# Kernel optimization log

Hardware: AMD Instinct MI355X
Metric: run time of the kernel (lower is better)

The kernel has to match this reference:

```python
import jax, jax.numpy as jnp
import numpy as np

B, N = 8192, 512
WEIGHT_THRESHOLD = 0.0
EPS = 1e-5


def setup_inputs() -> dict:
    key = jax.random.key(0)
    k1, k2, k3 = jax.random.split(key, 3)
    src_points = jax.random.normal(k1, (B, N, 3), dtype=jnp.float32)
    tgt_points = jax.random.normal(k2, (B, N, 3), dtype=jnp.float32)
    weights = jax.random.uniform(k3, (B, N), dtype=jnp.float32)
    return {"src_points": src_points, "tgt_points": tgt_points, "weights": weights}


def _weighted_procrustes(src, tgt, w):
    # threshold + normalize weights  (B, N)
    w = jnp.where(w < WEIGHT_THRESHOLD, jnp.zeros_like(w), w)
    w = w / (jnp.sum(w, axis=1, keepdims=True) + EPS)
    w3 = w[..., None]                                   # (B, N, 1)
    # weighted centroids (B, 1, 3)
    src_c = jnp.sum(w3 * src, axis=1, keepdims=True)
    tgt_c = jnp.sum(w3 * tgt, axis=1, keepdims=True)
    src0 = src - src_c
    tgt0 = tgt - tgt_c
    # weighted covariance H = src0^T (w * tgt0)  -> (B, 3, 3)
    H = jnp.einsum("bni,bnj->bij", src0, w3 * tgt0)
    U, S, Vh = jnp.linalg.svd(H)
    V = jnp.swapaxes(Vh, -1, -2)
    Ut = jnp.swapaxes(U, -1, -2)
    # reflection correction: diag(1, 1, sign(det(V U^T)))
    det = jnp.linalg.det(jnp.matmul(V, Ut))             # (B,)
    ones = jnp.ones((src.shape[0], 2), dtype=src.dtype)
    d = jnp.concatenate([ones, jnp.sign(det)[:, None]], axis=1)  # (B, 3)
    R = jnp.einsum("bij,bj,bjk->bik", V, d, Ut)         # (B, 3, 3)
    t = tgt_c[:, 0, :] - jnp.einsum("bij,bj->bi", R, src_c[:, 0, :])  # (B, 3)
    return R, t


def reference(src_points, tgt_points, weights):
    return _weighted_procrustes(src_points, tgt_points, weights)
```

## Files before the change

### kernel.cpp

```cpp
#include <hip/hip_runtime.h>

#define NPTS 512
#define BLOCK 256
#define BLOCK_S 64
#define XPS 68

#define GLOBAL_AS(p) ((const __attribute__((address_space(1))) void*)(p))
#define LDS_AS(p)    ((__attribute__((address_space(3))) void*)(p))

__global__ __launch_bounds__(BLOCK) void wproc_moments(
    const float* __restrict__ src,
    const float* __restrict__ tgt,
    const float* __restrict__ wts,
    float* __restrict__ ws)
{
    const int b = blockIdx.x;
    const int t = threadIdx.x;
    const int wave = t >> 6, lane = t & 63;

    __shared__ __align__(16) char smem[4 * 16 * XPS * 4];
    __shared__ float red[4][16];

    const char* sb = (const char*)(src + (size_t)b * (NPTS * 3));
    const char* tb = (const char*)(tgt + (size_t)b * (NPTS * 3));
    const char* wb = (const char*)(wts + (size_t)b * NPTS);

    for (int c = wave; c < 14; c += 4) {
        const char* g;
        if (c < 6)       g = sb + (size_t)c * 1024;
        else if (c < 12) g = tb + (size_t)(c - 6) * 1024;
        else             g = wb + (size_t)(c - 12) * 1024;
        __builtin_amdgcn_global_load_lds(
            GLOBAL_AS(g + lane * 16),
            LDS_AS(smem + c * 1024),
            16, 0, 2);
    }
    __syncthreads();

    const float* s_s = (const float*)smem;
    const float* s_t = (const float*)(smem + 6144);
    const float* s_w = (const float*)(smem + 12288);

    float acc[16];
    #pragma unroll
    for (int i = 0; i < 16; ++i) acc[i] = 0.f;

    #pragma unroll
    for (int k = 0; k < 2; ++k) {
        const int p = t + k * 256;
        float w = s_w[p];
        w = (w < 0.f) ? 0.f : w;
        const float sx = s_s[3 * p + 0], sy = s_s[3 * p + 1], sz = s_s[3 * p + 2];
        const float tx = s_t[3 * p + 0], ty = s_t[3 * p + 1], tz = s_t[3 * p + 2];
        acc[0] += w;
        acc[1] += w * sx; acc[2] += w * sy; acc[3] += w * sz;
        acc[4] += w * tx; acc[5] += w * ty; acc[6] += w * tz;
        const float wsx = w * sx, wsy = w * sy, wsz = w * sz;
        acc[7]  += wsx * tx; acc[8]  += wsx * ty; acc[9]  += wsx * tz;
        acc[10] += wsy * tx; acc[11] += wsy * ty; acc[12] += wsy * tz;
        acc[13] += wsz * tx; acc[14] += wsz * ty; acc[15] += wsz * tz;
    }
    __syncthreads();

    float (*xp)[16][XPS] = (float (*)[16][XPS])smem;
    #pragma unroll
    for (int m = 0; m < 16; ++m) xp[wave][m][lane] = acc[m];

    {
        const int m = lane & 15, q = lane >> 4;
        const float4* row = (const float4*)&xp[wave][m][0] + 4 * q;
        float4 a0 = row[0], a1 = row[1], a2 = row[2], a3 = row[3];
        a0.x += a1.x; a0.y += a1.y; a0.z += a1.z; a0.w += a1.w;
        a2.x += a3.x; a2.y += a3.y; a2.z += a3.z; a2.w += a3.w;
        a0.x += a2.x; a0.y += a2.y; a0.z += a2.z; a0.w += a2.w;
        float v = (a0.x + a0.y) + (a0.z + a0.w);
        v += __shfl_xor(v, 16, 64);
        v += __shfl_xor(v, 32, 64);
        if (q == 0) red[wave][m] = v;
    }
    __syncthreads();

    if (t < 16) {
        ws[(size_t)b * 16 + t] =
            (red[0][t] + red[1][t]) + (red[2][t] + red[3][t]);
    }
}

__global__ __launch_bounds__(BLOCK_S) void wproc_solve(
    const float* __restrict__ ws,
    float* __restrict__ out,
    int B)
{
    const int b = blockIdx.x * BLOCK_S + threadIdx.x;
    if (b >= B) return;

    double m[16];
    #pragma unroll
    for (int i = 0; i < 16; ++i) m[i] = (double)ws[(size_t)b * 16 + i];

    const double T = m[0] + 1e-5;
    const double f = 2.0 - m[0] / T;
    const double cs[3] = { m[1] / T, m[2] / T, m[3] / T };
    const double ct[3] = { m[4] / T, m[5] / T, m[6] / T };
    double H[3][3];
    #pragma unroll
    for (int i = 0; i < 3; ++i)
        #pragma unroll
        for (int j = 0; j < 3; ++j)
            H[i][j] = m[7 + i * 3 + j] / T - f * cs[i] * ct[j];

    double A[3][3];
    #pragma unroll
    for (int i = 0; i < 3; ++i)
        #pragma unroll
        for (int j = 0; j < 3; ++j)
            A[i][j] = H[0][i] * H[0][j] + H[1][i] * H[1][j] + H[2][i] * H[2][j];

    double V[3][3] = { {1, 0, 0}, {0, 1, 0}, {0, 0, 1} };
    #pragma unroll
    for (int sweep = 0; sweep < 5; ++sweep) {
        #pragma unroll
        for (int pair = 0; pair < 3; ++pair) {
            const int p = (pair == 2) ? 1 : 0;
            const int q = (pair == 0) ? 1 : 2;
            const double apq = A[p][q];
            const double theta = (A[q][q] - A[p][p]) / (2.0 * apq);
            const double tt = ((theta >= 0.0) ? 1.0 : -1.0)
                            / (fabs(theta) + sqrt(theta * theta + 1.0));
            double c  = 1.0 / sqrt(tt * tt + 1.0);
            double sn = tt * c;
            const bool zero = (apq == 0.0);
            c  = zero ? 1.0 : c;
            sn = zero ? 0.0 : sn;
            #pragma unroll
            for (int k = 0; k < 3; ++k) {
                const double akp = A[k][p], akq = A[k][q];
                A[k][p] = c * akp - sn * akq;
                A[k][q] = sn * akp + c * akq;
            }
            #pragma unroll
            for (int k = 0; k < 3; ++k) {
                const double apk = A[p][k], aqk = A[q][k];
                A[p][k] = c * apk - sn * aqk;
                A[q][k] = sn * apk + c * aqk;
            }
            #pragma unroll
            for (int k = 0; k < 3; ++k) {
                const double vkp = V[k][p], vkq = V[k][q];
                V[k][p] = c * vkp - sn * vkq;
                V[k][q] = sn * vkp + c * vkq;
            }
        }
    }

    double lam[3] = { A[0][0], A[1][1], A[2][2] };
    #define CSWAP(a_, b_) do {                                                \
        const bool sw_ = lam[a_] < lam[b_];                                   \
        const double tl_ = lam[a_];                                           \
        lam[a_] = sw_ ? lam[b_] : lam[a_];                                    \
        lam[b_] = sw_ ? tl_ : lam[b_];                                        \
        _Pragma("unroll")                                                     \
        for (int k = 0; k < 3; ++k) {                                         \
            const double tv_ = V[k][a_];                                      \
            V[k][a_] = sw_ ? V[k][b_] : V[k][a_];                             \
            V[k][b_] = sw_ ? tv_ : V[k][b_];                                  \
        }                                                                     \
    } while (0)
    CSWAP(0, 1); CSWAP(0, 2); CSWAP(1, 2);
    #undef CSWAP

    const double v1[3] = { V[0][0], V[1][0], V[2][0] };
    const double v2[3] = { V[0][1], V[1][1], V[2][1] };
    const double v3[3] = { v1[1] * v2[2] - v1[2] * v2[1],
                           v1[2] * v2[0] - v1[0] * v2[2],
                           v1[0] * v2[1] - v1[1] * v2[0] };

    double u1[3], u2[3], u3[3];
    #pragma unroll
    for (int i = 0; i < 3; ++i)
        u1[i] = H[i][0] * v1[0] + H[i][1] * v1[1] + H[i][2] * v1[2];
    double n1 = sqrt(u1[0] * u1[0] + u1[1] * u1[1] + u1[2] * u1[2]);
    n1 = (n1 > 1e-30) ? n1 : 1e-30;
    #pragma unroll
    for (int i = 0; i < 3; ++i) u1[i] /= n1;

    #pragma unroll
    for (int i = 0; i < 3; ++i)
        u2[i] = H[i][0] * v2[0] + H[i][1] * v2[1] + H[i][2] * v2[2];
    const double d12 = u1[0] * u2[0] + u1[1] * u2[1] + u1[2] * u2[2];
    #pragma unroll
    for (int i = 0; i < 3; ++i) u2[i] -= d12 * u1[i];
    double n2 = sqrt(u2[0] * u2[0] + u2[1] * u2[1] + u2[2] * u2[2]);
    n2 = (n2 > 1e-30) ? n2 : 1e-30;
    #pragma unroll
    for (int i = 0; i < 3; ++i) u2[i] /= n2;

    u3[0] = u1[1] * u2[2] - u1[2] * u2[1];
    u3[1] = u1[2] * u2[0] - u1[0] * u2[2];
    u3[2] = u1[0] * u2[1] - u1[1] * u2[0];

    double R[3][3];
    #pragma unroll
    for (int i = 0; i < 3; ++i)
        #pragma unroll
        for (int j = 0; j < 3; ++j)
            R[i][j] = v1[i] * u1[j] + v2[i] * u2[j] + v3[i] * u3[j];

    double tv[3];
    #pragma unroll
    for (int i = 0; i < 3; ++i)
        tv[i] = ct[i] - (R[i][0] * cs[0] + R[i][1] * cs[1] + R[i][2] * cs[2]);

    float* outR = out + (size_t)b * 9;
    #pragma unroll
    for (int i = 0; i < 3; ++i)
        #pragma unroll
        for (int j = 0; j < 3; ++j)
            outR[i * 3 + j] = (float)R[i][j];
    float* outT = out + (size_t)B * 9 + (size_t)b * 3;
    #pragma unroll
    for (int i = 0; i < 3; ++i) outT[i] = (float)tv[i];
}

extern "C" void kernel_launch(void* const* d_in, const int* in_sizes, int n_in,
                              void* d_out, int out_size, void* d_ws, size_t ws_size,
                              hipStream_t stream) {
    const float* src = (const float*)d_in[0];
    const float* tgt = (const float*)d_in[1];
    const float* wts = (const float*)d_in[2];
    float* out = (float*)d_out;
    float* ws = (float*)d_ws;
    const int B = out_size / 12;

    wproc_moments<<<B, BLOCK, 0, stream>>>(src, tgt, wts, ws);
    wproc_solve<<<(B + BLOCK_S - 1) / BLOCK_S, BLOCK_S, 0, stream>>>(ws, out, B);
}
```

Measured before the change: 134.6 us.

## Use persistent blocks with double-buffered async LDS staging in moments kernel

Replaces the one-block-per-batch moments kernel with a fixed grid of persistent blocks that loop over batches. Each iteration issues async global-to-LDS loads for the next batch into a second buffer while reducing the current one, so load latency overlaps compute. The cost is fewer resident blocks and extra LDS per block. A single barrier per iteration guards buffer reuse, and the xp scratch is reused between iterations, which raises questions about whether the LDS hazards are fully covered.

```diff
diff --git a/kernel.cpp b/kernel.cpp
--- a/kernel.cpp
+++ b/kernel.cpp
@@ -4,6 +4,7 @@
 #define BLOCK 256
 #define BLOCK_S 64
 #define XPS 68
+#define GRID_M 768
 
 #define GLOBAL_AS(p) ((const __attribute__((address_space(1))) void*)(p))
 #define LDS_AS(p)    ((__attribute__((address_space(3))) void*)(p))
@@ -12,77 +13,86 @@
     const float* __restrict__ src,
     const float* __restrict__ tgt,
     const float* __restrict__ wts,
-    float* __restrict__ ws)
+    float* __restrict__ ws,
+    int B)
 {
-    const int b = blockIdx.x;
     const int t = threadIdx.x;
     const int wave = t >> 6, lane = t & 63;
 
-    __shared__ __align__(16) char smem[4 * 16 * XPS * 4];
-    __shared__ float red[4][16];
-
-    const char* sb = (const char*)(src + (size_t)b * (NPTS * 3));
-    const char* tb = (const char*)(tgt + (size_t)b * (NPTS * 3));
-    const char* wb = (const char*)(wts + (size_t)b * NPTS);
-
-    for (int c = wave; c < 14; c += 4) {
-        const char* g;
-        if (c < 6)       g = sb + (size_t)c * 1024;
-        else if (c < 12) g = tb + (size_t)(c - 6) * 1024;
-        else             g = wb + (size_t)(c - 12) * 1024;
-        __builtin_amdgcn_global_load_lds(
-            GLOBAL_AS(g + lane * 16),
-            LDS_AS(smem + c * 1024),
-            16, 0, 2);
-    }
+    __shared__ __align__(16) char buf[2][14336];
+    __shared__ __align__(16) float xp[4][16][XPS];
+    __shared__ float red[2][4][16];
+
+    auto stage = [&](int b, char* dst) {
+        const char* sb = (const char*)(src + (size_t)b * (NPTS * 3));
+        const char* tb = (const char*)(tgt + (size_t)b * (NPTS * 3));
+        const char* wb = (const char*)(wts + (size_t)b * NPTS);
+        for (int c = wave; c < 14; c += 4) {
+            const char* g;
+            if (c < 6)       g = sb + (size_t)c * 1024;
+            else if (c < 12) g = tb + (size_t)(c - 6) * 1024;
+            else             g = wb + (size_t)(c - 12) * 1024;
+            __builtin_amdgcn_global_load_lds(
+                GLOBAL_AS(g + lane * 16),
+                LDS_AS(dst + c * 1024),
+                16, 0, 2);
+        }
+    };
+
+    int b = blockIdx.x;
+    if (b < B) stage(b, buf[0]);
     __syncthreads();
 
-    const float* s_s = (const float*)smem;
-    const float* s_t = (const float*)(smem + 6144);
-    const float* s_w = (const float*)(smem + 12288);
-
-    float acc[16];
-    #pragma unroll
-    for (int i = 0; i < 16; ++i) acc[i] = 0.f;
-
-    #pragma unroll
-    for (int k = 0; k < 2; ++k) {
-        const int p = t + k * 256;
-        float w = s_w[p];
-        w = (w < 0.f) ? 0.f : w;
-        const float sx = s_s[3 * p + 0], sy = s_s[3 * p + 1], sz = s_s[3 * p + 2];
-        const float tx = s_t[3 * p + 0], ty = s_t[3 * p + 1], tz = s_t[3 * p + 2];
-        acc[0] += w;
-        acc[1] += w * sx; acc[2] += w * sy; acc[3] += w * sz;
-        acc[4] += w * tx; acc[5] += w * ty; acc[6] += w * tz;
-        const float wsx = w * sx, wsy = w * sy, wsz = w * sz;
-        acc[7]  += wsx * tx; acc[8]  += wsx * ty; acc[9]  += wsx * tz;
-        acc[10] += wsy * tx; acc[11] += wsy * ty; acc[12] += wsy * tz;
-        acc[13] += wsz * tx; acc[14] += wsz * ty; acc[15] += wsz * tz;
-    }
-    __syncthreads();
-
-    float (*xp)[16][XPS] = (float (*)[16][XPS])smem;
-    #pragma unroll
-    for (int m = 0; m < 16; ++m) xp[wave][m][lane] = acc[m];
-
-    {
-        const int m = lane & 15, q = lane >> 4;
-        const float4* row = (const float4*)&xp[wave][m][0] + 4 * q;
-        float4 a0 = row[0], a1 = row[1], a2 = row[2], a3 = row[3];
-        a0.x += a1.x; a0.y += a1.y; a0.z += a1.z; a0.w += a1.w;
-        a2.x += a3.x; a2.y += a3.y; a2.z += a3.z; a2.w += a3.w;
-        a0.x += a2.x; a0.y += a2.y; a0.z += a2.z; a0.w += a2.w;
-        float v = (a0.x + a0.y) + (a0.z + a0.w);
-        v += __shfl_xor(v, 16, 64);
-        v += __shfl_xor(v, 32, 64);
-        if (q == 0) red[wave][m] = v;
-    }
-    __syncthreads();
-
-    if (t < 16) {
-        ws[(size_t)b * 16 + t] =
-            (red[0][t] + red[1][t]) + (red[2][t] + red[3][t]);
+    int p = 0;
+    for (; b < B; b += GRID_M, p ^= 1) {
+        const int bn = b + GRID_M;
+        if (bn < B) stage(bn, buf[p ^ 1]);
+
+        const float* s_s = (const float*)(buf[p]);
+        const float* s_t = (const float*)(buf[p] + 6144);
+        const float* s_w = (const float*)(buf[p] + 12288);
+
+        float acc[16];
+        #pragma unroll
+        for (int j = 0; j < 16; ++j) acc[j] = 0.f;
+
+        #pragma unroll
+        for (int k = 0; k < 2; ++k) {
+            const int pt = t + k * 256;
+            float w = s_w[pt];
+            w = (w < 0.f) ? 0.f : w;
+            const float sx = s_s[3 * pt + 0], sy = s_s[3 * pt + 1], sz = s_s[3 * pt + 2];
+            const float tx = s_t[3 * pt + 0], ty = s_t[3 * pt + 1], tz = s_t[3 * pt + 2];
+            acc[0] += w;
+            acc[1] += w * sx; acc[2] += w * sy; acc[3] += w * sz;
+            acc[4] += w * tx; acc[5] += w * ty; acc[6] += w * tz;
+            const float wsx = w * sx, wsy = w * sy, wsz = w * sz;
+            acc[7]  += wsx * tx; acc[8]  += wsx * ty; acc[9]  += wsx * tz;
+            acc[10] += wsy * tx; acc[11] += wsy * ty; acc[12] += wsy * tz;
+            acc[13] += wsz * tx; acc[14] += wsz * ty; acc[15] += wsz * tz;
+        }
+
+        #pragma unroll
+        for (int mI = 0; mI < 16; ++mI) xp[wave][mI][lane] = acc[mI];
+        {
+            const int mI = lane & 15, q = lane >> 4;
+            const float4* row = (const float4*)&xp[wave][mI][0] + 4 * q;
+            float4 a0 = row[0], a1 = row[1], a2 = row[2], a3 = row[3];
+            a0.x += a1.x; a0.y += a1.y; a0.z += a1.z; a0.w += a1.w;
+            a2.x += a3.x; a2.y += a3.y; a2.z += a3.z; a2.w += a3.w;
+            a0.x += a2.x; a0.y += a2.y; a0.z += a2.z; a0.w += a2.w;
+            float v = (a0.x + a0.y) + (a0.z + a0.w);
+            v += __shfl_xor(v, 16, 64);
+            v += __shfl_xor(v, 32, 64);
+            if (q == 0) red[p][wave][mI] = v;
+        }
+
+        __syncthreads();
+
+        if (t < 16) {
+            ws[(size_t)b * 16 + t] =
+                (red[p][0][t] + red[p][1][t]) + (red[p][2][t] + red[p][3][t]);
+        }
     }
 }
 
@@ -232,6 +242,6 @@
     float* ws = (float*)d_ws;
     const int B = out_size / 12;
 
-    wproc_moments<<<B, BLOCK, 0, stream>>>(src, tgt, wts, ws);
+    wproc_moments<<<GRID_M, BLOCK, 0, stream>>>(src, tgt, wts, ws, B);
     wproc_solve<<<(B + BLOCK_S - 1) / BLOCK_S, BLOCK_S, 0, stream>>>(ws, out, B);
 }
```

Result: slower. 139.6 us (+3.7%).
